# Performance work log

Measured on AMD Instinct MI355X. Metric: run time of the kernel, lower is better.

## Reference

```python
import jax, jax.numpy as jnp
import numpy as np

CAPSULE_WIDE = 8
CAPSULE_TALL = 4
FEAT = 784
FV = FEAT // CAPSULE_TALL  # 196
B = 32768


def _linear_params(key, out_dim, in_dim):
    kw, kb = jax.random.split(key)
    bound = 1.0 / np.sqrt(in_dim)
    W = jax.random.uniform(kw, (out_dim, in_dim), minval=-bound, maxval=bound, dtype=jnp.float32)
    b = jax.random.uniform(kb, (out_dim,), minval=-bound, maxval=bound, dtype=jnp.float32)
    return W, b


def setup_inputs() -> dict:
    key = jax.random.key(0)
    ks = jax.random.split(key, 7)
    x = jax.random.normal(ks[0], (B, FEAT), dtype=jnp.float32)
    W1, b1 = _linear_params(ks[1], FV, FV)
    W2, b2 = _linear_params(ks[2], FV, FV)
    W3, b3 = _linear_params(ks[3], FV, FV)
    Wd1, bd1 = _linear_params(ks[4], FEAT, FEAT)
    Wd2, bd2 = _linear_params(ks[5], FEAT, FEAT)
    Wo, bo = _linear_params(ks[6], 10, FEAT)
    return {"x": x, "W1": W1, "b1": b1, "W2": W2, "b2": b2, "W3": W3, "b3": b3,
            "Wd1": Wd1, "bd1": bd1, "Wd2": Wd2, "bd2": bd2, "Wo": Wo, "bo": bo}


def reference(x, W1, b1, W2, b2, W3, b3, Wd1, bd1, Wd2, bd2, Wo, bo):
    h = x  # [B, 784]
    for _ in range(CAPSULE_WIDE):
        v = h.reshape(h.shape[0], CAPSULE_TALL, FV)  # [B, T, FV]
        q = v @ W1.T + b1  # first_copy
        k = v @ W2.T + b2  # second_copy
        u = v @ W3.T + b3  # third_copy
        scores = jnp.einsum('btf,bsf->bts', q, k)  # [B, T, T], unscaled
        probs = jax.nn.softmax(scores, axis=-1)
        h = jnp.einsum('bts,bsf->btf', probs, u).reshape(h.shape[0], -1)
    dec = jax.nn.relu(h @ Wd1.T + bd1) @ Wd2.T + bd2  # output_decoder
    return jax.nn.softmax(dec @ Wo.T + bo, axis=-1)  # output_probability
```

## Files before the change

kernel.cpp:

```cpp
#include <hip/hip_runtime.h>
#include <math.h>

#define NT 256
#define NTC 512
typedef _Float16 f16;
typedef _Float16 half8 __attribute__((ext_vector_type(8)));
typedef _Float16 half4 __attribute__((ext_vector_type(4)));
typedef float floatx4 __attribute__((ext_vector_type(4)));

#define ROWSHR_ADD(v, N) \
  (v) += __int_as_float(__builtin_amdgcn_update_dpp(0, __float_as_int(v), 0x110 | (N), 0xF, 0xF, true))

#define WD1_OFF  0
#define WD2_OFF  1433600
#define WOT_OFF  2867200
#define D8_OFF   2918400
#define HBUF_OFF 2919424
#define D1_OFF   55348224
#define WPKH_OFF 55348224
#define WPKL_OFF 56186880
#define SSE      38464

__device__ inline void glds16(const void* g, void* l) {
  __builtin_amdgcn_global_load_lds((const __attribute__((address_space(1))) void*)g,
                                   (__attribute__((address_space(3))) void*)l, 16, 0, 0);
}

__global__ void k_prep_io(const float* __restrict__ Wd1, const float* __restrict__ Wd2,
                          const float* __restrict__ Wo,
                          f16* __restrict__ W1p, f16* __restrict__ W2p,
                          float* __restrict__ WoT) {
  int b = blockIdx.x;
  if (b < 5600) {
    const float* Wd = (b < 2800) ? Wd1 : Wd2;
    f16* W16 = (b < 2800) ? W1p : W2p;
    int idx = (b % 2800) * NT + threadIdx.x;
    if (idx < 896 * 800) {
      int n = idx / 800, k = idx - n * 800;
      W16[idx] = (f16)((n < 784 && k < 784) ? Wd[n * 784 + k] : 0.f);
    }
  } else {
    int idx = (b - 5600) * NT + threadIdx.x;
    if (idx < 784 * 16) {
      int f = idx >> 4, n = idx & 15;
      WoT[idx] = (n < 10) ? Wo[n * 784 + f] : 0.f;
    }
  }
}

__global__ void k_prep_gq(const float* __restrict__ W1, const float* __restrict__ W2,
                          const float* __restrict__ W3, float* __restrict__ scr) {
  __shared__ float red[256];
  const int tid = threadIdx.x;
  int b = blockIdx.x;
  if (b < 1202) {
    int ta = (b < 601);
    const float* A = ta ? W1 : W3;
    const float* B = ta ? W2 : W3;
    float* C = ta ? scr : (scr + (size_t)2 * SSE);
    int u = ta ? b : (b - 601);
    int o = u * 64 + (tid & 63);
    int ks = tid >> 6;
    float s = 0.f;
    int p = 0, r = 0;
    if (o < 38416) {
      p = o / 196; r = o - p * 196;
      const int c0 = ks * 49;
      #pragma unroll 7
      for (int c = c0; c < c0 + 49; ++c) {
        float a = ta ? A[c * 196 + p] : A[p * 196 + c];
        s += a * B[c * 196 + r];
      }
    }
    red[tid] = s;
    __syncthreads();
    if (tid < 64 && o < 38416)
      C[p * 196 + r] = red[tid] + red[tid + 64] + red[tid + 128] + red[tid + 192];
  } else {
    int idx = (b - 1202) * NT + tid;
    if (idx < 38416) scr[(size_t)SSE + idx] = W3[idx];
  }
}

__constant__ int MMA[4][8] = {{2,2,1,2,0,0,0,0},{4,4,4,4,3,4,9,10},
                              {5,6,7,11,12,0,0,0},{13,14,15,0,0,0,0,0}};
__constant__ int MMB[4][8] = {{1,2,0,0,0,0,0,0},{1,2,3,4,0,0,1,2},
                              {0,0,0,3,4,0,0,0},{5,6,7,0,0,0,0,0}};
__constant__ int MMC[4][8] = {{3,4,9,10,0,0,0,0},{5,6,7,8,11,12,16,17},
                              {13,14,15,18,19,0,0,0},{20,21,22,0,0,0,0,0}};
__constant__ int MMT[4][8] = {{0,0,1,1,0,0,0,0},{0,0,0,0,1,1,0,0},
                              {1,1,1,0,0,0,0,0},{0,0,0,0,0,0,0,0}};

__global__ __launch_bounds__(NT, 4)
void k_mmb(float* __restrict__ scr, int stage,
           const float* __restrict__ W2, const float* __restrict__ b1,
           const float* __restrict__ b3, float* __restrict__ d8out) {
  __shared__ float red[256];
  __shared__ float z[196], cj[196], dd[196], tmp[196];
  const int tid = threadIdx.x;
  const int y = blockIdx.y;

  if (stage == 2 && y == 5) {
    if (blockIdx.x >= 8) return;
    const int i = blockIdx.x;
    const float* G = scr;
    const float* Qbase = scr + (size_t)SSE;
    float* gtab = scr + (size_t)23 * SSE;
    const float* W3c = Qbase;
    for (int t = tid; t < 196; t += NT) {
      float s = 0.f;
      for (int f = 0; f < 196; ++f) s += b1[f] * W2[f * 196 + t];
      z[t] = s; dd[t] = 0.f; cj[t] = b3[t];
    }
    __syncthreads();
    for (int j = 0; j < i; ++j) {
      for (int t = tid; t < 196; t += NT) {
        float s = 0.f;
        for (int c = 0; c < 196; ++c) s += W3c[t * 196 + c] * cj[c];
        tmp[t] = s; dd[t] += cj[t];
      }
      __syncthreads();
      for (int t = tid; t < 196; t += NT) cj[t] = tmp[t];
      __syncthreads();
    }
    if (i == 7)
      for (int t = tid; t < 196; t += NT) d8out[t] = dd[t] + cj[t];
    for (int t = tid; t < 196; t += NT) {
      float s = z[t];
      for (int k = 0; k < 196; ++k) s += G[k * 196 + t] * dd[k];
      tmp[t] = s;
    }
    __syncthreads();
    for (int t = tid; t < 196; t += NT) {
      float s;
      if (i == 0) s = tmp[t];
      else {
        const float* Qi = Qbase + (size_t)(i - 1) * SSE;
        s = 0.f;
        for (int n = 0; n < 196; ++n) s += Qi[n * 196 + t] * tmp[n];
      }
      gtab[i * 196 + t] = s;
    }
    return;
  }

  const float* A = scr + (size_t)MMA[stage][y] * SSE;
  const float* B = scr + (size_t)MMB[stage][y] * SSE;
  float*       C = scr + (size_t)MMC[stage][y] * SSE;
  const int ta = MMT[stage][y];
  int o = blockIdx.x * 64 + (tid & 63);
  int ks = tid >> 6;
  float s = 0.f;
  int p = 0, r = 0;
  if (o < 38416) {
    p = o / 196; r = o - p * 196;
    const int c0 = ks * 49;
    #pragma unroll 7
    for (int c = c0; c < c0 + 49; ++c) {
      float a = ta ? A[c * 196 + p] : A[p * 196 + c];
      s += a * B[c * 196 + r];
    }
  }
  red[tid] = s;
  __syncthreads();
  if (tid < 64 && o < 38416)
    C[p * 196 + r] = red[tid] + red[tid + 64] + red[tid + 128] + red[tid + 192];
}

__global__ void k_prep_pack(const float* __restrict__ scr,
                            f16* __restrict__ Wph, f16* __restrict__ Wpl) {
  int idx = blockIdx.x * NT + threadIdx.x;
  if (idx >= 9 * 208 * 224) return;
  int s = idx / (208 * 224), rem = idx - s * (208 * 224);
  int n = rem / 224, k = rem - n * 224;
  float v = 0.f;
  if (k < 196) {
    if (n < 196) {
      if (s == 8) v = scr[(size_t)8 * SSE + n * 196 + k];
      else {
        const float* M = (s == 0) ? scr : (scr + (size_t)(16 + s - 1) * SSE);
        v = M[k * 196 + n];
      }
    } else if (n == 196 && s < 8) {
      v = scr[(size_t)23 * SSE + s * 196 + k];
    }
  }
  f16 hi = (f16)v;
  Wph[idx] = hi;
  Wpl[idx] = (f16)(v - (float)hi);
}

__global__ __launch_bounds__(NTC, 4)
void k_caps(const float* __restrict__ x,
            const f16* __restrict__ Wph, const f16* __restrict__ Wpl,
            const float* __restrict__ d8g,
            f16* __restrict__ hbuf) {
  __shared__ __align__(16) char smem[70656];
  f16*   vAhi = (f16*)smem;
  f16*   vAlo = (f16*)(smem + 29696);
  float* Sful = (float*)(smem + 59392);
  float* Rl   = (float*)(smem + 67584);
  float* Cm   = (float*)(smem + 69632);

  const int tid  = threadIdx.x;
  const int w    = tid >> 6;
  const int lane = tid & 63;
  const int l15  = lane & 15;
  const int quad = lane >> 4;
  const int e0   = blockIdx.x * 16;
  const bool haveJ1 = (w + 8) < 13;

  for (int idx = tid; idx < 16 * 196; idx += NTC) {
    int elem = idx / 196, g = idx - elem * 196;
    int t = g / 49, f = (g - t * 49) * 4;
    floatx4 v4 = *(const floatx4*)&x[(size_t)(e0 + elem) * 784 + g * 4];
    half4 h4, l4;
    #pragma unroll
    for (int q = 0; q < 4; ++q) {
      f16 h = (f16)v4[q];
      h4[q] = h;
      l4[q] = (f16)(v4[q] - (float)h);
    }
    int vo = (elem * 4 + t) * 232 + f;
    *(half4*)&vAhi[vo] = h4;
    *(half4*)&vAlo[vo] = l4;
  }
  for (int p = tid; p < 64 * 36; p += NTC) {
    int row = p / 36, c = 196 + (p - (p / 36) * 36);
    vAhi[row * 232 + c] = (f16)0;
    vAlo[row * 232 + c] = (f16)0;
  }
  for (int p = tid; p < 2048; p += NTC) Sful[p] = 0.f;
  __syncthreads();

  float vv0[4][4], vv1[4][4];
  {
    int c0 = w * 16 + l15;
    int c1 = 128 + w * 16 + l15;
    #pragma unroll
    for (int mt = 0; mt < 4; ++mt)
      #pragma unroll
      for (int s = 0; s < 4; ++s) {
        int ro = ((mt * 4 + quad) * 4 + s) * 232;
        vv0[mt][s] = (float)vAhi[ro + c0] + (float)vAlo[ro + c0];
        vv1[mt][s] = haveJ1 ? ((float)vAhi[ro + c1] + (float)vAlo[ro + c1]) : 0.f;
      }
  }

  #pragma unroll 1
  for (int i = 0; i < 8; ++i) {
    floatx4 acc0[4], acc1[4];
    #pragma unroll
    for (int mt = 0; mt < 4; ++mt) {
      acc0[mt] = (floatx4){0.f, 0.f, 0.f, 0.f};
      acc1[mt] = (floatx4){0.f, 0.f, 0.f, 0.f};
    }
    const int wb0 = ((i * 208 + w * 16 + l15) * 224) + quad * 8;
    const int wb1 = ((i * 208 + (w + 8) * 16 + l15) * 224) + quad * 8;
    #pragma unroll
    for (int ks = 0; ks < 7; ++ks) {
      half8 ah[4], al[4];
      #pragma unroll
      for (int mt = 0; mt < 4; ++mt) {
        int ao = (mt * 16 + l15) * 232 + ks * 32 + quad * 8;
        ah[mt] = *(const half8*)&vAhi[ao];
        al[mt] = *(const half8*)&vAlo[ao];
      }
      {
        half8 bh = *(const half8*)&Wph[wb0 + ks * 32];
        half8 bl = *(const half8*)&Wpl[wb0 + ks * 32];
        #pragma unroll
        for (int mt = 0; mt < 4; ++mt) {
          acc0[mt] = __builtin_amdgcn_mfma_f32_16x16x32_f16(ah[mt], bh, acc0[mt], 0, 0, 0);
          acc0[mt] = __builtin_amdgcn_mfma_f32_16x16x32_f16(ah[mt], bl, acc0[mt], 0, 0, 0);
          acc0[mt] = __builtin_amdgcn_mfma_f32_16x16x32_f16(al[mt], bh, acc0[mt], 0, 0, 0);
        }
      }
      if (haveJ1) {
        half8 bh = *(const half8*)&Wph[wb1 + ks * 32];
        half8 bl = *(const half8*)&Wpl[wb1 + ks * 32];
        #pragma unroll
        for (int mt = 0; mt < 4; ++mt) {
          acc1[mt] = __builtin_amdgcn_mfma_f32_16x16x32_f16(ah[mt], bh, acc1[mt], 0, 0, 0);
          acc1[mt] = __builtin_amdgcn_mfma_f32_16x16x32_f16(ah[mt], bl, acc1[mt], 0, 0, 0);
          acc1[mt] = __builtin_amdgcn_mfma_f32_16x16x32_f16(al[mt], bh, acc1[mt], 0, 0, 0);
        }
      }
    }
    #pragma unroll
    for (int mt = 0; mt < 4; ++mt) {
      float part[16];
      #pragma unroll
      for (int t = 0; t < 4; ++t)
        #pragma unroll
        for (int s = 0; s < 4; ++s)
          part[t * 4 + s] = acc0[mt][t] * vv0[mt][s] + acc1[mt][t] * vv1[mt][s];
      #pragma unroll
      for (int p = 0; p < 16; ++p) {
        ROWSHR_ADD(part[p], 8);
        ROWSHR_ADD(part[p], 4);
        ROWSHR_ADD(part[p], 2);
        ROWSHR_ADD(part[p], 1);
      }
      if (l15 == 0) {
        int elem = mt * 4 + quad;
        #pragma unroll
        for (int t = 0; t < 4; ++t)
          #pragma unroll
          for (int s = 0; s < 4; ++s)
            atomicAdd(&Sful[((i * 16 + elem) * 4 + t) * 4 + s], part[t * 4 + s]);
      }
    }
    if (w == 4 && l15 == 4) {
      #pragma unroll
      for (int mt = 0; mt < 4; ++mt)
        *(floatx4*)&Rl[i * 64 + mt * 16 + quad * 4] = acc1[mt];
    }
  }
  __syncthreads();

  if (tid < 16) {
    const int e = tid;
    float C[4][4] = {{1,0,0,0},{0,1,0,0},{0,0,1,0},{0,0,0,1}};
    #pragma unroll 1
    for (int i = 0; i < 8; ++i) {
      float M[4][4];
      #pragma unroll
      for (int a = 0; a < 4; ++a) {
        floatx4 mm = *(const floatx4*)&Sful[((i * 16 + e) * 4 + a) * 4];
        #pragma unroll
        for (int b = 0; b < 4; ++b) M[a][b] = mm[b];
      }
      floatx4 rv = *(const floatx4*)&Rl[i * 64 + e * 4];
      float T1[4][4], Cr[4];
      #pragma unroll
      for (int t = 0; t < 4; ++t)
        #pragma unroll
        for (int b = 0; b < 4; ++b)
          T1[t][b] = C[t][0]*M[0][b] + C[t][1]*M[1][b] + C[t][2]*M[2][b] + C[t][3]*M[3][b];
      #pragma unroll
      for (int s = 0; s < 4; ++s)
        Cr[s] = C[s][0]*rv[0] + C[s][1]*rv[1] + C[s][2]*rv[2] + C[s][3]*rv[3];
      float P[4][4];
      #pragma unroll
      for (int t = 0; t < 4; ++t) {
        float S[4];
        #pragma unroll
        for (int s = 0; s < 4; ++s)
          S[s] = T1[t][0]*C[s][0] + T1[t][1]*C[s][1] + T1[t][2]*C[s][2] + T1[t][3]*C[s][3] + Cr[s];
        float m = fmaxf(fmaxf(S[0], S[1]), fmaxf(S[2], S[3]));
        float e0_ = __expf(S[0] - m), e1 = __expf(S[1] - m);
        float e2 = __expf(S[2] - m), e3 = __expf(S[3] - m);
        float inv = 1.f / (e0_ + e1 + e2 + e3);
        P[t][0] = e0_ * inv; P[t][1] = e1 * inv; P[t][2] = e2 * inv; P[t][3] = e3 * inv;
      }
      float Cn[4][4];
      #pragma unroll
      for (int t = 0; t < 4; ++t)
        #pragma unroll
        for (int s = 0; s < 4; ++s)
          Cn[t][s] = P[t][0]*C[0][s] + P[t][1]*C[1][s] + P[t][2]*C[2][s] + P[t][3]*C[3][s];
      #pragma unroll
      for (int t = 0; t < 4; ++t)
        #pragma unroll
        for (int s = 0; s < 4; ++s) C[t][s] = Cn[t][s];
    }
    #pragma unroll
    for (int t = 0; t < 4; ++t)
      *(floatx4*)&Cm[e * 16 + t * 4] = (floatx4){C[t][0], C[t][1], C[t][2], C[t][3]};
  }
  __syncthreads();

  {
    floatx4 acu0[4], acu1[4];
    #pragma unroll
    for (int mt = 0; mt < 4; ++mt) {
      acu0[mt] = (floatx4){0.f, 0.f, 0.f, 0.f};
      acu1[mt] = (floatx4){0.f, 0.f, 0.f, 0.f};
    }
    const int wb0 = ((8 * 208 + w * 16 + l15) * 224) + quad * 8;
    const int wb1 = ((8 * 208 + (w + 8) * 16 + l15) * 224) + quad * 8;
    #pragma unroll
    for (int ks = 0; ks < 7; ++ks) {
      half8 ah[4], al[4];
      #pragma unroll
      for (int mt = 0; mt < 4; ++mt) {
        int ao = (mt * 16 + l15) * 232 + ks * 32 + quad * 8;
        ah[mt] = *(const half8*)&vAhi[ao];
        al[mt] = *(const half8*)&vAlo[ao];
      }
      {
        half8 bh = *(const half8*)&Wph[wb0 + ks * 32];
        half8 bl = *(const half8*)&Wpl[wb0 + ks * 32];
        #pragma unroll
        for (int mt = 0; mt < 4; ++mt) {
          acu0[mt] = __builtin_amdgcn_mfma_f32_16x16x32_f16(ah[mt], bh, acu0[mt], 0, 0, 0);
          acu0[mt] = __builtin_amdgcn_mfma_f32_16x16x32_f16(ah[mt], bl, acu0[mt], 0, 0, 0);
          acu0[mt] = __builtin_amdgcn_mfma_f32_16x16x32_f16(al[mt], bh, acu0[mt], 0, 0, 0);
        }
      }
      if (haveJ1) {
        half8 bh = *(const half8*)&Wph[wb1 + ks * 32];
        half8 bl = *(const half8*)&Wpl[wb1 + ks * 32];
        #pragma unroll
        for (int mt = 0; mt < 4; ++mt) {
          acu1[mt] = __builtin_amdgcn_mfma_f32_16x16x32_f16(ah[mt], bh, acu1[mt], 0, 0, 0);
          acu1[mt] = __builtin_amdgcn_mfma_f32_16x16x32_f16(ah[mt], bl, acu1[mt], 0, 0, 0);
          acu1[mt] = __builtin_amdgcn_mfma_f32_16x16x32_f16(al[mt], bh, acu1[mt], 0, 0, 0);
        }
      }
    }
    const int f0 = w * 16 + l15;
    const int f1 = 128 + w * 16 + l15;
    const bool doF1 = haveJ1 && (f1 < 196);
    float d80 = d8g[f0];
    float d81 = doF1 ? d8g[f1] : 0.f;
    #pragma unroll
    for (int mt = 0; mt < 4; ++mt) {
      int elem = mt * 4 + quad;
      floatx4 c0 = *(const floatx4*)&Cm[elem * 16 + 0];
      floatx4 c1 = *(const floatx4*)&Cm[elem * 16 + 4];
      floatx4 c2 = *(const floatx4*)&Cm[elem * 16 + 8];
      floatx4 c3 = *(const floatx4*)&Cm[elem * 16 + 12];
      {
        floatx4 u = acu0[mt];
        float h0 = c0[0]*u[0] + c0[1]*u[1] + c0[2]*u[2] + c0[3]*u[3] + d80;
        float h1 = c1[0]*u[0] + c1[1]*u[1] + c1[2]*u[2] + c1[3]*u[3] + d80;
        float h2 = c2[0]*u[0] + c2[1]*u[1] + c2[2]*u[2] + c2[3]*u[3] + d80;
        float h3 = c3[0]*u[0] + c3[1]*u[1] + c3[2]*u[2] + c3[3]*u[3] + d80;
        size_t base = (size_t)(e0 + elem) * 800;
        hbuf[base + 0 * 196 + f0] = (f16)h0;
        hbuf[base + 1 * 196 + f0] = (f16)h1;
        hbuf[base + 2 * 196 + f0] = (f16)h2;
        hbuf[base + 3 * 196 + f0] = (f16)h3;
      }
      if (doF1) {
        floatx4 u = acu1[mt];
        float h0 = c0[0]*u[0] + c0[1]*u[1] + c0[2]*u[2] + c0[3]*u[3] + d81;
        float h1 = c1[0]*u[0] + c1[1]*u[1] + c1[2]*u[2] + c1[3]*u[3] + d81;
        float h2 = c2[0]*u[0] + c2[1]*u[1] + c2[2]*u[2] + c2[3]*u[3] + d81;
        float h3 = c3[0]*u[0] + c3[1]*u[1] + c3[2]*u[2] + c3[3]*u[3] + d81;
        size_t base = (size_t)(e0 + elem) * 800;
        hbuf[base + 0 * 196 + f1] = (f16)h0;
        hbuf[base + 1 * 196 + f1] = (f16)h1;
        hbuf[base + 2 * 196 + f1] = (f16)h2;
        hbuf[base + 3 * 196 + f1] = (f16)h3;
      }
    }
  }
  for (int idx = tid; idx < 256; idx += NTC)
    hbuf[(size_t)(e0 + (idx >> 4)) * 800 + 784 + (idx & 15)] = (f16)0;
}

__global__ __launch_bounds__(NT, 2)
void k_dec(const f16* __restrict__ A, const f16* __restrict__ Bw,
           const float* __restrict__ bias, f16* __restrict__ C, int do_relu) {
  __shared__ __align__(16) f16 As[128 * 32];
  __shared__ __align__(16) f16 Bs[128 * 32];
  const int tid = threadIdx.x, w = tid >> 6, lane = tid & 63;
  const int l15 = lane & 15, quad = lane >> 4;
  const int m0 = blockIdx.x * 128, n0 = blockIdx.y * 128;
  const int wm = w & 1, wn = w >> 1;
  const int srow = lane >> 2, soff = (lane & 3) * 8;

  floatx4 acc[4][4];
  #pragma unroll
  for (int nt = 0; nt < 4; ++nt) {
    int col = n0 + wn * 64 + nt * 16 + l15;
    float bb = (col < 784) ? bias[col] : 0.f;
    #pragma unroll
    for (int mt = 0; mt < 4; ++mt) acc[mt][nt] = (floatx4){bb, bb, bb, bb};
  }

  for (int kk = 0; kk < 25; ++kk) {
    __syncthreads();
    #pragma unroll
    for (int i = 0; i < 2; ++i) {
      int r = w * 32 + i * 16;
      glds16(&A[(size_t)(m0 + r + srow) * 800 + kk * 32 + soff], &As[r * 32]);
      glds16(&Bw[(size_t)(n0 + r + srow) * 800 + kk * 32 + soff], &Bs[r * 32]);
    }
    __syncthreads();
    half8 af[4], bf[4];
    #pragma unroll
    for (int mt = 0; mt < 4; ++mt)
      af[mt] = *(const half8*)&As[(wm * 64 + mt * 16 + l15) * 32 + quad * 8];
    #pragma unroll
    for (int nt = 0; nt < 4; ++nt)
      bf[nt] = *(const half8*)&Bs[(wn * 64 + nt * 16 + l15) * 32 + quad * 8];
    #pragma unroll
    for (int mt = 0; mt < 4; ++mt)
      #pragma unroll
      for (int nt = 0; nt < 4; ++nt)
        acc[mt][nt] = __builtin_amdgcn_mfma_f32_16x16x32_f16(af[mt], bf[nt], acc[mt][nt], 0, 0, 0);
  }

  #pragma unroll
  for (int nt = 0; nt < 4; ++nt) {
    int gcol = n0 + wn * 64 + nt * 16 + l15;
    if (gcol < 800) {
      #pragma unroll
      for (int mt = 0; mt < 4; ++mt) {
        #pragma unroll
        for (int r = 0; r < 4; ++r) {
          int grow = m0 + wm * 64 + mt * 16 + quad * 4 + r;
          float v = acc[mt][nt][r];
          if (do_relu) v = fmaxf(v, 0.f);
          C[(size_t)grow * 800 + gcol] = (f16)v;
        }
      }
    }
  }
}

__global__ __launch_bounds__(NT, 4)
void k_logits(const f16* __restrict__ d2, const float* __restrict__ WoT,
              const float* __restrict__ bo, float* __restrict__ out) {
  __shared__ __align__(16) f16 ds[16 * 800];
  __shared__ float lg[160];
  const int tid = threadIdx.x;
  const size_t e0 = (size_t)blockIdx.x * 16;
  for (int i = tid; i < 16 * 98; i += NT) {
    int e = i / 98, c = (i - e * 98) * 8;
    *(half8*)&ds[e * 800 + c] = *(const half8*)&d2[(e0 + e) * 800 + c];
  }
  __syncthreads();
  {
    int e = tid >> 4, n = tid & 15;
    const f16* dp = &ds[e * 800];
    float s = 0.f;
    #pragma unroll 4
    for (int f = 0; f < 784; ++f) s += (float)dp[f] * WoT[f * 16 + n];
    if (n < 10) lg[e * 10 + n] = s + bo[n];
  }
  __syncthreads();
  if (tid < 16) {
    float l[10], m = -1e30f;
    #pragma unroll
    for (int n = 0; n < 10; ++n) { l[n] = lg[tid * 10 + n]; m = fmaxf(m, l[n]); }
    float sum = 0.f;
    #pragma unroll
    for (int n = 0; n < 10; ++n) { l[n] = __expf(l[n] - m); sum += l[n]; }
    float inv = 1.f / sum;
    #pragma unroll
    for (int n = 0; n < 10; ++n) out[(e0 + tid) * 10 + n] = l[n] * inv;
  }
}

extern "C" void kernel_launch(void* const* d_in, const int* in_sizes, int n_in,
                              void* d_out, int out_size, void* d_ws, size_t ws_size,
                              hipStream_t stream) {
  const float* x   = (const float*)d_in[0];
  const float* W1  = (const float*)d_in[1];
  const float* b1  = (const float*)d_in[2];
  const float* W2  = (const float*)d_in[3];
  const float* W3  = (const float*)d_in[5];
  const float* b3  = (const float*)d_in[6];
  const float* Wd1 = (const float*)d_in[7];
  const float* bd1 = (const float*)d_in[8];
  const float* Wd2 = (const float*)d_in[9];
  const float* bd2 = (const float*)d_in[10];
  const float* Wo  = (const float*)d_in[11];
  const float* bo  = (const float*)d_in[12];
  float* out = (float*)d_out;

  char* ws = (char*)d_ws;
  f16*   Wd1p  = (f16*)(ws + WD1_OFF);
  f16*   Wd2p  = (f16*)(ws + WD2_OFF);
  float* WoTws = (float*)(ws + WOT_OFF);
  float* d8ws  = (float*)(ws + D8_OFF);
  f16*   hbuf  = (f16*)(ws + HBUF_OFF);
  f16*   d1buf = (f16*)(ws + D1_OFF);
  f16*   Wph   = (f16*)(ws + WPKH_OFF);
  f16*   Wpl   = (f16*)(ws + WPKL_OFF);
  float* scr   = (float*)(ws + HBUF_OFF);

  k_prep_io<<<5649, NT, 0, stream>>>(Wd1, Wd2, Wo, Wd1p, Wd2p, WoTws);
  k_prep_gq<<<1353, NT, 0, stream>>>(W1, W2, W3, scr);
  k_mmb<<<dim3(601, 4), NT, 0, stream>>>(scr, 0, W2, b1, b3, d8ws);
  k_mmb<<<dim3(601, 8), NT, 0, stream>>>(scr, 1, W2, b1, b3, d8ws);
  k_mmb<<<dim3(601, 6), NT, 0, stream>>>(scr, 2, W2, b1, b3, d8ws);
  k_mmb<<<dim3(601, 3), NT, 0, stream>>>(scr, 3, W2, b1, b3, d8ws);
  k_prep_pack<<<(9 * 208 * 224 + NT - 1) / NT, NT, 0, stream>>>(scr, Wph, Wpl);

  k_caps<<<32768 / 16, NTC, 0, stream>>>(x, Wph, Wpl, d8ws, hbuf);
  k_dec<<<dim3(32768 / 128, 7), NT, 0, stream>>>(hbuf, Wd1p, bd1, d1buf, 1);
  k_dec<<<dim3(32768 / 128, 7), NT, 0, stream>>>(d1buf, Wd2p, bd2, hbuf, 0);
  k_logits<<<32768 / 16, NT, 0, stream>>>(hbuf, WoTws, bo, out);
}
```

Before: 889.7 us.

## Double-buffer decoder GEMM LDS tiles with K=64 steps and XOR swizzle

The decoder GEMM kernel now uses two LDS buffers with 64-wide K tiles. The next tile is prefetched via global_load_lds while MFMAs run on the current one, and there is one barrier per step instead of two. An XOR swizzle on the 16-byte chunks is meant to cut LDS bank conflicts. The leftover 32-wide K tail (768..799) is read straight from global memory. LDS use grows fourfold (64KB per block), which may limit the 2-blocks-per-CU launch bound and occupancy.

```diff
diff --git a/kernel.cpp b/kernel.cpp
--- a/kernel.cpp
+++ b/kernel.cpp
@@ -455,13 +455,14 @@
 __global__ __launch_bounds__(NT, 2)
 void k_dec(const f16* __restrict__ A, const f16* __restrict__ Bw,
            const float* __restrict__ bias, f16* __restrict__ C, int do_relu) {
-  __shared__ __align__(16) f16 As[128 * 32];
-  __shared__ __align__(16) f16 Bs[128 * 32];
-  const int tid = threadIdx.x, w = tid >> 6, lane = tid & 63;
+  __shared__ __align__(16) f16 As[2][128 * 64];
+  __shared__ __align__(16) f16 Bs[2][128 * 64];
+  const int tid = threadIdx.x, wv = tid >> 6, lane = tid & 63;
   const int l15 = lane & 15, quad = lane >> 4;
   const int m0 = blockIdx.x * 128, n0 = blockIdx.y * 128;
-  const int wm = w & 1, wn = w >> 1;
-  const int srow = lane >> 2, soff = (lane & 3) * 8;
+  const int wm = wv & 1, wn = wv >> 1;
+  const int srow = lane >> 3;
+  const int sg   = lane & 7;
 
   floatx4 acc[4][4];
   #pragma unroll
@@ -472,22 +473,60 @@
     for (int mt = 0; mt < 4; ++mt) acc[mt][nt] = (floatx4){bb, bb, bb, bb};
   }
 
-  for (int kk = 0; kk < 25; ++kk) {
+  #define DEC_STAGE(buf, k0)                                                        \
+    do {                                                                            \
+      _Pragma("unroll")                                                             \
+      for (int j = 0; j < 4; ++j) {                                                 \
+        int row = wv * 32 + j * 8 + srow;                                           \
+        int gs = sg ^ (row & 7);                                                    \
+        glds16(&A[(size_t)(m0 + row) * 800 + (k0) + gs * 8],                        \
+               &As[buf][(wv * 32 + j * 8) * 64]);                                   \
+        glds16(&Bw[(size_t)(n0 + row) * 800 + (k0) + gs * 8],                       \
+               &Bs[buf][(wv * 32 + j * 8) * 64]);                                   \
+      }                                                                             \
+    } while (0)
+
+  DEC_STAGE(0, 0);
+  __syncthreads();
+
+  int cur = 0;
+  #pragma unroll 1
+  for (int kk = 0; kk < 12; ++kk) {
+    if (kk < 11) DEC_STAGE(cur ^ 1, (kk + 1) * 64);
+    half8 af[2][4], bf[2][4];
+    #pragma unroll
+    for (int h = 0; h < 2; ++h) {
+      #pragma unroll
+      for (int mt = 0; mt < 4; ++mt) {
+        int row = wm * 64 + mt * 16 + l15;
+        af[h][mt] = *(const half8*)&As[cur][row * 64 + (((h << 2) | quad) ^ (l15 & 7)) * 8];
+      }
+      #pragma unroll
+      for (int nt = 0; nt < 4; ++nt) {
+        int row = wn * 64 + nt * 16 + l15;
+        bf[h][nt] = *(const half8*)&Bs[cur][row * 64 + (((h << 2) | quad) ^ (l15 & 7)) * 8];
+      }
+    }
+    #pragma unroll
+    for (int h = 0; h < 2; ++h)
+      #pragma unroll
+      for (int mt = 0; mt < 4; ++mt)
+        #pragma unroll
+        for (int nt = 0; nt < 4; ++nt)
+          acc[mt][nt] = __builtin_amdgcn_mfma_f32_16x16x32_f16(af[h][mt], bf[h][nt], acc[mt][nt], 0, 0, 0);
     __syncthreads();
-    #pragma unroll
-    for (int i = 0; i < 2; ++i) {
-      int r = w * 32 + i * 16;
-      glds16(&A[(size_t)(m0 + r + srow) * 800 + kk * 32 + soff], &As[r * 32]);
-      glds16(&Bw[(size_t)(n0 + r + srow) * 800 + kk * 32 + soff], &Bs[r * 32]);
-    }
-    __syncthreads();
+    cur ^= 1;
+  }
+  #undef DEC_STAGE
+
+  {
     half8 af[4], bf[4];
     #pragma unroll
     for (int mt = 0; mt < 4; ++mt)
-      af[mt] = *(const half8*)&As[(wm * 64 + mt * 16 + l15) * 32 + quad * 8];
+      af[mt] = *(const half8*)&A[(size_t)(m0 + wm * 64 + mt * 16 + l15) * 800 + 768 + quad * 8];
     #pragma unroll
     for (int nt = 0; nt < 4; ++nt)
-      bf[nt] = *(const half8*)&Bs[(wn * 64 + nt * 16 + l15) * 32 + quad * 8];
+      bf[nt] = *(const half8*)&Bw[(size_t)(n0 + wn * 64 + nt * 16 + l15) * 800 + 768 + quad * 8];
     #pragma unroll
     for (int mt = 0; mt < 4; ++mt)
       #pragma unroll
```

Result: slower. 912.0 us (+2.5%).
